# Optimization experiments

Hardware: AMD Instinct MI355X
Metric: run time of the kernel (lower is better)

Reference implementation:

```python
import jax, jax.numpy as jnp
import numpy as np


def setup_inputs() -> dict:
    key = jax.random.key(0)
    k1, k2, k3, k4 = jax.random.split(key, 4)
    B, T, L, C, F = 1024, 128, 256, 2, 784
    x = jax.random.normal(k1, (B, T, F), dtype=jnp.float32)
    W = jax.random.normal(k2, (L, F), dtype=jnp.float32) * (1.0 / np.sqrt(F))
    b = jax.random.normal(k3, (L,), dtype=jnp.float32) * 0.01
    contribution = jax.random.normal(k4, (T, L, C), dtype=jnp.float32)
    return {"x": x, "W": W, "b": b, "contribution": contribution}


def reference(x, W, b, contribution):
    # symbolic_paths: Linear(784 -> leaf) + Hardtanh  -> [B, T, L]
    sp = jnp.clip(jnp.einsum('btf,lf->btl', x, W) + b, -1.0, 1.0)
    # per-(tree,leaf) outer product: class_value[b,t,l,c] = sp[b,t,l] * contribution[t,l,c]
    cv = sp[..., None] * contribution[None]          # [B, T, L, C]
    p = jax.nn.softmax(cv, axis=-1)                  # softmax over classes
    gini = jnp.sum(1.0 - p * p, axis=-1)             # [B, T, L]
    return (sp, gini)
```

## Files before the change

kernel.cpp:

```cpp
#include <hip/hip_runtime.h>
#include <hip/hip_bf16.h>

typedef __attribute__((ext_vector_type(8))) short bf16x8;
typedef __attribute__((ext_vector_type(4))) float f32x4;

#define B_SZ   1024
#define T_SZ   128
#define L_SZ   256
#define F_SZ   784
#define M_TOT  (B_SZ * T_SZ)
#define BK     32
#define KSTEPS 25

#define WPRE_ELEMS (KSTEPS * 4 * L_SZ)
#define WPRE_BYTES (WPRE_ELEMS * 16)
#define CDIFF_ELEMS (T_SZ * L_SZ)
#define WS_NEED (WPRE_BYTES + CDIFF_ELEMS * 4)

#define ROWB   656
#define WINB   (32 * ROWB)
#define BUFB   21504

__device__ __forceinline__ unsigned short f2bf(float f) {
    __hip_bfloat16 h = __float2bfloat16(f);
    return *reinterpret_cast<unsigned short*>(&h);
}

__global__ __launch_bounds__(256) void dn_prep(
    const float* __restrict__ W, const float* __restrict__ contrib,
    unsigned short* __restrict__ wpre, float* __restrict__ cdiff)
{
    const int gid = blockIdx.x * 256 + threadIdx.x;
    if (gid < WPRE_ELEMS) {
        const int leaf = gid & 255;
        const int kg   = (gid >> 8) & 3;
        const int ks   = gid >> 10;
        const int k0   = ks * BK + kg * 8;
        bf16x8 v;
        #pragma unroll
        for (int j = 0; j < 8; ++j) {
            const int k = k0 + j;
            const float f = (k < F_SZ) ? W[(size_t)leaf * F_SZ + k] : 0.f;
            v[j] = (short)f2bf(f);
        }
        *reinterpret_cast<bf16x8*>(wpre + (size_t)gid * 8) = v;
    } else {
        const int cid = gid - WPRE_ELEMS;
        if (cid < CDIFF_ELEMS)
            cdiff[cid] = contrib[(size_t)cid * 2] - contrib[(size_t)cid * 2 + 1];
    }
}


#define GLDS(g, l)                                                           \
    __builtin_amdgcn_global_load_lds(                                        \
        (const __attribute__((address_space(1))) void*)(g),                  \
        (__attribute__((address_space(3))) void*)(l), 16, 0, 0)

__global__ __launch_bounds__(512, 6) void dn_fused12(
    const float* __restrict__ x, const unsigned short* __restrict__ wpre,
    const float* __restrict__ bias, const float* __restrict__ cdiff,
    float* __restrict__ out)
{
    __shared__ __align__(16) unsigned char smem[2 * BUFB];

    const int tid  = threadIdx.x;
    const int lane = tid & 63;
    const int wid  = tid >> 6;
    const int lr   = lane & 15;
    const int kseg = lane >> 4;

    const int rowBase = blockIdx.x * 32;
    const int colBase = wid * 32;

    const char* xb = (const char*)x;
    const char* srcB[3];
    const char* srcC[3];
    bool        v4[3];
    #pragma unroll
    for (int jj = 0; jj < 3; ++jj) {
        const int j = wid + 8 * jj;
        const unsigned s    = j * 1024 + lane * 16;
        const unsigned row  = s / ROWB;
        const unsigned colb = s - row * ROWB;
        const bool     ok   = (row < 32) && (colb < 640);
        const unsigned rcl  = (row < 32) ? row : 0;
        srcC[jj] = xb + (size_t)(rowBase + rcl) * 3136;
        srcB[jj] = srcC[jj] + (ok ? colb : 0);
        v4[jj]   = ok && (colb < 576);
    }

    #define ISSUE(w) do {                                                    \
        _Pragma("unroll")                                                    \
        for (int _jj = 0; _jj < 3; ++_jj) {                                  \
            const int _j = wid + 8 * _jj;                                    \
            if (_j < 21) {                                                   \
                const char* _s = ((w) < 4) ? (srcB[_jj] + (w) * 640)         \
                                : (v4[_jj] ? srcB[_jj] + 2560 : srcC[_jj]);  \
                GLDS(_s, smem + ((w) & 1) * BUFB + _j * 1024);               \
            }                                                                \
        }                                                                    \
    } while (0)

    f32x4 acc[2][2];
    #pragma unroll
    for (int mi = 0; mi < 2; ++mi)
        #pragma unroll
        for (int ni = 0; ni < 2; ++ni)
            acc[mi][ni] = (f32x4){0.f, 0.f, 0.f, 0.f};

    const unsigned short* wpb = wpre + ((size_t)kseg * L_SZ + colBase + lr) * 8;
    bf16x8 wcur[2], wnxt[2];

    ISSUE(0);
    wcur[0] = *reinterpret_cast<const bf16x8*>(wpb);
    wcur[1] = *reinterpret_cast<const bf16x8*>(wpb + 128);
    asm volatile("s_waitcnt vmcnt(0)" ::: "memory");
    __builtin_amdgcn_s_barrier();

    #pragma unroll
    for (int w = 0; w < 5; ++w) {
        if (w < 4) ISSUE(w + 1);

        const unsigned char* Ab = smem + (w & 1) * BUFB;
        #pragma unroll
        for (int i = 0; i < 5; ++i) {
            const int ks = w * 5 + i;
            if (ks + 1 < KSTEPS) {
                wnxt[0] = *reinterpret_cast<const bf16x8*>(wpb + (size_t)(ks + 1) * 8192);
                wnxt[1] = *reinterpret_cast<const bf16x8*>(wpb + (size_t)(ks + 1) * 8192 + 128);
            }
            bf16x8 af[2];
            #pragma unroll
            for (int m = 0; m < 2; ++m) {
                const int off = (m * 16 + lr) * ROWB + i * 128 + kseg * 32;
                const f32x4 alo = *reinterpret_cast<const f32x4*>(Ab + off);
                const f32x4 ahi = *reinterpret_cast<const f32x4*>(Ab + off + 16);
                #pragma unroll
                for (int jd = 0; jd < 4; ++jd) {
                    af[m][jd]     = (short)f2bf(alo[jd]);
                    af[m][4 + jd] = (short)f2bf(ahi[jd]);
                }
            }
            acc[0][0] = __builtin_amdgcn_mfma_f32_16x16x32_bf16(af[0], wcur[0], acc[0][0], 0, 0, 0);
            acc[0][1] = __builtin_amdgcn_mfma_f32_16x16x32_bf16(af[0], wcur[1], acc[0][1], 0, 0, 0);
            acc[1][0] = __builtin_amdgcn_mfma_f32_16x16x32_bf16(af[1], wcur[0], acc[1][0], 0, 0, 0);
            acc[1][1] = __builtin_amdgcn_mfma_f32_16x16x32_bf16(af[1], wcur[1], acc[1][1], 0, 0, 0);
            wcur[0] = wnxt[0];
            wcur[1] = wnxt[1];
        }
        asm volatile("s_waitcnt vmcnt(0)" ::: "memory");
        __builtin_amdgcn_sched_barrier(0);
        __builtin_amdgcn_s_barrier();
    }
    #undef ISSUE

    float spv[2][2][4];
    #pragma unroll
    for (int ni = 0; ni < 2; ++ni) {
        const float bb = bias[colBase + ni * 16 + lr];
        #pragma unroll
        for (int mi = 0; mi < 2; ++mi)
            #pragma unroll
            for (int r = 0; r < 4; ++r)
                spv[mi][ni][r] = fminf(fmaxf(acc[mi][ni][r] + bb, -1.f), 1.f);
    }

    typedef float OtRow[264];
    OtRow* Ot = reinterpret_cast<OtRow*>(smem);

    const int erow = tid >> 4;
    const int ecol = (tid & 15) * 4;
    const size_t GOFF = (size_t)M_TOT * L_SZ;
    float* orow = out + (size_t)(rowBase + erow) * L_SZ;

    #pragma unroll
    for (int ni = 0; ni < 2; ++ni)
        #pragma unroll
        for (int mi = 0; mi < 2; ++mi)
            #pragma unroll
            for (int r = 0; r < 4; ++r)
                Ot[mi * 16 + kseg * 4 + r][colBase + ni * 16 + lr] = spv[mi][ni][r];
    __syncthreads();
    #pragma unroll
    for (int j = 0; j < 4; ++j) {
        const f32x4 v = *reinterpret_cast<const f32x4*>(&Ot[erow][ecol + 64 * j]);
        *reinterpret_cast<f32x4*>(orow + ecol + 64 * j) = v;
    }
    __syncthreads();

    #pragma unroll
    for (int ni = 0; ni < 2; ++ni) {
        const int col = colBase + ni * 16 + lr;
        #pragma unroll
        for (int mi = 0; mi < 2; ++mi)
            #pragma unroll
            for (int r = 0; r < 4; ++r) {
                const int t = (rowBase + mi * 16 + kseg * 4 + r) & (T_SZ - 1);
                const float d  = spv[mi][ni][r] * cdiff[t * L_SZ + col];
                const float ed = __expf(d);
                const float s2 = ed / (1.f + ed);
                Ot[mi * 16 + kseg * 4 + r][col] = fmaf(2.f * s2, 1.f - s2, 1.f);
            }
    }
    __syncthreads();
    #pragma unroll
    for (int j = 0; j < 4; ++j) {
        const f32x4 v = *reinterpret_cast<const f32x4*>(&Ot[erow][ecol + 64 * j]);
        *reinterpret_cast<f32x4*>(orow + GOFF + ecol + 64 * j) = v;
    }
}

__global__ __launch_bounds__(512) void dn_fused_v1(
    const float* __restrict__ x, const float* __restrict__ W,
    const float* __restrict__ bias, const float* __restrict__ contrib,
    float* __restrict__ out)
{
    __shared__ bf16x8 As[4][128];
    __shared__ bf16x8 Bs[4][L_SZ];

    const int tid    = threadIdx.x;
    const int lane   = tid & 63;
    const int wid    = tid >> 6;
    const int waveM  = wid >> 2;
    const int waveN  = wid & 3;
    const int blkRow = blockIdx.x * 128;
    const int ar = tid >> 2;
    const int ak = (tid & 3) * 8;
    const int wr = tid >> 1;
    const int wk = (tid & 1) * 16;
    const int laneRow = lane & 15;
    const int kgrp    = lane >> 4;

    f32x4 acc[4][4];
    #pragma unroll
    for (int i = 0; i < 4; ++i)
        #pragma unroll
        for (int j = 0; j < 4; ++j)
            acc[i][j] = (f32x4){0.f, 0.f, 0.f, 0.f};

    const float* xrow = x + (size_t)(blkRow + ar) * F_SZ;
    const float* wrow = W + (size_t)wr * F_SZ;
    const f32x4 zf = {0.f, 0.f, 0.f, 0.f};

    f32x4 xa0 = *reinterpret_cast<const f32x4*>(xrow + ak);
    f32x4 xa1 = *reinterpret_cast<const f32x4*>(xrow + ak + 4);
    f32x4 wa0 = *reinterpret_cast<const f32x4*>(wrow + wk);
    f32x4 wa1 = *reinterpret_cast<const f32x4*>(wrow + wk + 4);
    f32x4 wa2 = *reinterpret_cast<const f32x4*>(wrow + wk + 8);
    f32x4 wa3 = *reinterpret_cast<const f32x4*>(wrow + wk + 12);

    for (int ks = 0; ks < KSTEPS; ++ks) {
        bf16x8 av, wv0, wv1;
        #pragma unroll
        for (int j = 0; j < 4; ++j) {
            av[j]      = (short)f2bf(xa0[j]);
            av[4 + j]  = (short)f2bf(xa1[j]);
            wv0[j]     = (short)f2bf(wa0[j]);
            wv0[4 + j] = (short)f2bf(wa1[j]);
            wv1[j]     = (short)f2bf(wa2[j]);
            wv1[4 + j] = (short)f2bf(wa3[j]);
        }
        As[ak >> 3][ar] = av;
        Bs[wk >> 3][wr] = wv0;
        Bs[(wk >> 3) + 1][wr] = wv1;
        __syncthreads();

        if (ks + 1 < KSTEPS) {
            const int kb = (ks + 1) * BK;
            if (kb + ak < F_SZ) {
                xa0 = *reinterpret_cast<const f32x4*>(xrow + kb + ak);
                xa1 = *reinterpret_cast<const f32x4*>(xrow + kb + ak + 4);
            } else { xa0 = zf; xa1 = zf; }
            if (kb + wk < F_SZ) {
                wa0 = *reinterpret_cast<const f32x4*>(wrow + kb + wk);
                wa1 = *reinterpret_cast<const f32x4*>(wrow + kb + wk + 4);
                wa2 = *reinterpret_cast<const f32x4*>(wrow + kb + wk + 8);
                wa3 = *reinterpret_cast<const f32x4*>(wrow + kb + wk + 12);
            } else { wa0 = zf; wa1 = zf; wa2 = zf; wa3 = zf; }
        }

        bf16x8 af[4], bfv[4];
        #pragma unroll
        for (int mi = 0; mi < 4; ++mi)
            af[mi] = As[kgrp][waveM * 64 + mi * 16 + laneRow];
        #pragma unroll
        for (int ni = 0; ni < 4; ++ni)
            bfv[ni] = Bs[kgrp][waveN * 64 + ni * 16 + laneRow];
        #pragma unroll
        for (int mi = 0; mi < 4; ++mi)
            #pragma unroll
            for (int ni = 0; ni < 4; ++ni)
                acc[mi][ni] = __builtin_amdgcn_mfma_f32_16x16x32_bf16(
                    af[mi], bfv[ni], acc[mi][ni], 0, 0, 0);
        __syncthreads();
    }

    const size_t GOFF  = (size_t)M_TOT * L_SZ;
    const int    rbase = waveM * 64 + (lane >> 4) * 4;
    const int    cbase = waveN * 64 + laneRow;
    #pragma unroll
    for (int ni = 0; ni < 4; ++ni) {
        const int col = cbase + ni * 16;
        const float bb = bias[col];
        #pragma unroll
        for (int mi = 0; mi < 4; ++mi) {
            #pragma unroll
            for (int r = 0; r < 4; ++r) {
                const int m = blkRow + rbase + mi * 16 + r;
                const int t = m & (T_SZ - 1);
                float v  = acc[mi][ni][r] + bb;
                float sp = fminf(fmaxf(v, -1.f), 1.f);
                const float* cp = contrib + (size_t)(t * L_SZ + col) * 2;
                const float d  = sp * (cp[0] - cp[1]);
                const float ed = __expf(d);
                const float s  = ed / (1.f + ed);
                const float g  = fmaf(2.f * s, 1.f - s, 1.f);
                const size_t o = (size_t)m * L_SZ + col;
                out[o]        = sp;
                out[GOFF + o] = g;
            }
        }
    }
}

extern "C" void kernel_launch(void* const* d_in, const int* in_sizes, int n_in,
                              void* d_out, int out_size, void* d_ws, size_t ws_size,
                              hipStream_t stream) {
    const float* x       = (const float*)d_in[0];
    const float* W       = (const float*)d_in[1];
    const float* bias    = (const float*)d_in[2];
    const float* contrib = (const float*)d_in[3];
    float* out = (float*)d_out;

    if (ws_size >= (size_t)WS_NEED && d_ws != nullptr) {
        unsigned short* wpre  = (unsigned short*)d_ws;
        float*          cdiff = (float*)((char*)d_ws + WPRE_BYTES);
        const int prep_threads = WPRE_ELEMS + CDIFF_ELEMS;
        dn_prep<<<(prep_threads + 255) / 256, 256, 0, stream>>>(W, contrib, wpre, cdiff);
        dn_fused12<<<M_TOT / 32, 512, 0, stream>>>(x, wpre, bias, cdiff, out);
    } else {
        dn_fused_v1<<<M_TOT / 128, 512, 0, stream>>>(x, W, bias, contrib, out);
    }
}
```

Before: 190.0 us.

## Convert A tile to bf16 once per block in shared memory

Each window of x is now converted from fp32 to bf16 cooperatively by the whole block into a separate bf16 LDS buffer, and the MFMA loop reads pre-converted fragments. Before, every wave converted the same A rows on its own. The fp32 staging becomes a single buffer: the next global-to-LDS load is issued after the conversion, so it overlaps the MFMA work. This adds two block barriers per window and serialises conversion with the load wait, while reducing LDS footprint.

Result: no change. 187.6 us (-1.2%).

```diff
diff --git a/kernel.cpp b/kernel.cpp
--- a/kernel.cpp
+++ b/kernel.cpp
@@ -17,9 +17,9 @@
 #define CDIFF_ELEMS (T_SZ * L_SZ)
 #define WS_NEED (WPRE_BYTES + CDIFF_ELEMS * 4)
 
-#define ROWB   656
-#define WINB   (32 * ROWB)
-#define BUFB   21504
+#define ROWB    656
+#define ABF_OFF 21504
+#define SMEM_SZ 33792
 
 __device__ __forceinline__ unsigned short f2bf(float f) {
     __hip_bfloat16 h = __float2bfloat16(f);
@@ -57,12 +57,12 @@
         (const __attribute__((address_space(1))) void*)(g),                  \
         (__attribute__((address_space(3))) void*)(l), 16, 0, 0)
 
-__global__ __launch_bounds__(512, 6) void dn_fused12(
+__global__ __launch_bounds__(512, 6) void dn_fused13(
     const float* __restrict__ x, const unsigned short* __restrict__ wpre,
     const float* __restrict__ bias, const float* __restrict__ cdiff,
     float* __restrict__ out)
 {
-    __shared__ __align__(16) unsigned char smem[2 * BUFB];
+    __shared__ __align__(16) unsigned char smem[SMEM_SZ];
 
     const int tid  = threadIdx.x;
     const int lane = tid & 63;
@@ -97,11 +97,34 @@
             if (_j < 21) {                                                   \
                 const char* _s = ((w) < 4) ? (srcB[_jj] + (w) * 640)         \
                                 : (v4[_jj] ? srcB[_jj] + 2560 : srcC[_jj]);  \
-                GLDS(_s, smem + ((w) & 1) * BUFB + _j * 1024);               \
+                GLDS(_s, smem + _j * 1024);                                  \
             }                                                                \
         }                                                                    \
     } while (0)
 
+    #define CVT() do {                                                       \
+        _Pragma("unroll")                                                    \
+        for (int _h = 0; _h < 2; ++_h) {                                     \
+            const int _c = tid + _h * 512;                                   \
+            if (_c < 640) {                                                  \
+                const int _row = _c / 20;                                    \
+                const int _kc  = _c - _row * 20;                             \
+                const f32x4 _lo = *reinterpret_cast<const f32x4*>(           \
+                    smem + _row * ROWB + _kc * 32);                          \
+                const f32x4 _hi = *reinterpret_cast<const f32x4*>(           \
+                    smem + _row * ROWB + _kc * 32 + 16);                     \
+                bf16x8 _v;                                                   \
+                _Pragma("unroll")                                            \
+                for (int _j = 0; _j < 4; ++_j) {                             \
+                    _v[_j]     = (short)f2bf(_lo[_j]);                       \
+                    _v[4 + _j] = (short)f2bf(_hi[_j]);                       \
+                }                                                            \
+                *reinterpret_cast<bf16x8*>(smem + ABF_OFF                    \
+                    + (_kc * 33 + _row) * 16) = _v;                          \
+            }                                                                \
+        }                                                                    \
+    } while (0)
+
     f32x4 acc[2][2];
     #pragma unroll
     for (int mi = 0; mi < 2; ++mi)
@@ -115,14 +138,13 @@
     ISSUE(0);
     wcur[0] = *reinterpret_cast<const bf16x8*>(wpb);
     wcur[1] = *reinterpret_cast<const bf16x8*>(wpb + 128);
-    asm volatile("s_waitcnt vmcnt(0)" ::: "memory");
-    __builtin_amdgcn_s_barrier();
+    __syncthreads();
+    CVT();
+    __syncthreads();
+    ISSUE(1);
 
     #pragma unroll
     for (int w = 0; w < 5; ++w) {
-        if (w < 4) ISSUE(w + 1);
-
-        const unsigned char* Ab = smem + (w & 1) * BUFB;
         #pragma unroll
         for (int i = 0; i < 5; ++i) {
             const int ks = w * 5 + i;
@@ -132,16 +154,10 @@
             }
             bf16x8 af[2];
             #pragma unroll
-            for (int m = 0; m < 2; ++m) {
-                const int off = (m * 16 + lr) * ROWB + i * 128 + kseg * 32;
-                const f32x4 alo = *reinterpret_cast<const f32x4*>(Ab + off);
-                const f32x4 ahi = *reinterpret_cast<const f32x4*>(Ab + off + 16);
-                #pragma unroll
-                for (int jd = 0; jd < 4; ++jd) {
-                    af[m][jd]     = (short)f2bf(alo[jd]);
-                    af[m][4 + jd] = (short)f2bf(ahi[jd]);
-                }
-            }
+            for (int m = 0; m < 2; ++m)
+                af[m] = *reinterpret_cast<const bf16x8*>(
+                    smem + ABF_OFF + (((i * 4 + kseg) * 33) + m * 16 + lr) * 16);
+
             acc[0][0] = __builtin_amdgcn_mfma_f32_16x16x32_bf16(af[0], wcur[0], acc[0][0], 0, 0, 0);
             acc[0][1] = __builtin_amdgcn_mfma_f32_16x16x32_bf16(af[0], wcur[1], acc[0][1], 0, 0, 0);
             acc[1][0] = __builtin_amdgcn_mfma_f32_16x16x32_bf16(af[1], wcur[0], acc[1][0], 0, 0, 0);
@@ -149,11 +165,15 @@
             wcur[0] = wnxt[0];
             wcur[1] = wnxt[1];
         }
-        asm volatile("s_waitcnt vmcnt(0)" ::: "memory");
-        __builtin_amdgcn_sched_barrier(0);
-        __builtin_amdgcn_s_barrier();
+        if (w < 4) {
+            __syncthreads();
+            CVT();
+            __syncthreads();
+            if (w < 3) ISSUE(w + 2);
+        }
     }
     #undef ISSUE
+    #undef CVT
 
     float spv[2][2][4];
     #pragma unroll
@@ -173,6 +193,8 @@
     const int ecol = (tid & 15) * 4;
     const size_t GOFF = (size_t)M_TOT * L_SZ;
     float* orow = out + (size_t)(rowBase + erow) * L_SZ;
+
+    __syncthreads();
 
     #pragma unroll
     for (int ni = 0; ni < 2; ++ni)
@@ -338,7 +360,7 @@
         float*          cdiff = (float*)((char*)d_ws + WPRE_BYTES);
         const int prep_threads = WPRE_ELEMS + CDIFF_ELEMS;
         dn_prep<<<(prep_threads + 255) / 256, 256, 0, stream>>>(W, contrib, wpre, cdiff);
-        dn_fused12<<<M_TOT / 32, 512, 0, stream>>>(x, wpre, bias, cdiff, out);
+        dn_fused13<<<M_TOT / 32, 512, 0, stream>>>(x, wpre, bias, cdiff, out);
     } else {
         dn_fused_v1<<<M_TOT / 128, 512, 0, stream>>>(x, W, bias, contrib, out);
     }
```
